# Kernel optimization log

Measured on AMD Instinct MI355X. Metric: run time of the kernel, lower is better.

The kernel has to match this reference:

```python
import jax, jax.numpy as jnp
import numpy as np

# Model dims (DeepSeek-V2-Lite-like MLA)
B, S, DIM, H = 2, 2048, 2048, 16
QR, KVR = 1536, 512          # q_lora_rank, kv_lora_rank
DN, DR, DV = 128, 64, 128    # qk_nope_head_dim, qk_rope_head_dim, v_head_dim
QKD = DN + DR                # qk_head_dim = 192
SCALE = QKD ** -0.5          # max_seq_len == original_seq_len -> no mscale correction
EPS = float(jnp.finfo(jnp.float32).eps)  # torch.nn.RMSNorm default eps


def rmsnorm(x, w):
    return x * jax.lax.rsqrt(jnp.mean(x * x, axis=-1, keepdims=True) + EPS) * w


def rope(x, cos, sin):
    # x: [B, S, H, D]; cos/sin: [S, D//2]. Matches torch.view_as_complex on
    # consecutive (real, imag) pairs, multiply by freqs_cis, flatten back.
    xr, xi = x[..., 0::2], x[..., 1::2]
    c = cos[None, :, None, :]
    s = sin[None, :, None, :]
    yr = xr * c - xi * s
    yi = xr * s + xi * c
    return jnp.stack([yr, yi], axis=-1).reshape(x.shape)


def _xavier(key, out_f, in_f):
    lim = (6.0 / (in_f + out_f)) ** 0.5
    return jax.random.uniform(key, (out_f, in_f), jnp.float32, -lim, lim)


def setup_inputs() -> dict:
    key = jax.random.key(0)
    ks = jax.random.split(key, 8)
    x = jax.random.normal(ks[0], (B, S, DIM), jnp.float32)
    # rotary tables: theta=10000, rope dim = DR
    inv = 1.0 / (10000.0 ** (np.arange(0, DR, 2, dtype=np.float64) / DR))
    ang = np.arange(S, dtype=np.float64)[:, None] * inv[None, :]
    freqs_cos = jnp.asarray(np.cos(ang), jnp.float32)
    freqs_sin = jnp.asarray(np.sin(ang), jnp.float32)
    # causal mask [S, S]: 0 on/below diagonal, -1e9 above
    idx = jnp.arange(S)
    mask = jnp.where(idx[:, None] >= idx[None, :], 0.0, -1e9).astype(jnp.float32)
    return {
        "x": x,
        "freqs_cos": freqs_cos,
        "freqs_sin": freqs_sin,
        "mask": mask,
        "wq_a_w": _xavier(ks[1], QR, DIM), "wq_a_b": jnp.zeros((QR,), jnp.float32),
        "q_norm_w": jnp.ones((QR,), jnp.float32),
        "wq_b_w": _xavier(ks[2], H * QKD, QR), "wq_b_b": jnp.zeros((H * QKD,), jnp.float32),
        "wkv_a_w": _xavier(ks[3], KVR + DR, DIM), "wkv_a_b": jnp.zeros((KVR + DR,), jnp.float32),
        "kv_norm_w": jnp.ones((KVR,), jnp.float32),
        "wkv_b_w": _xavier(ks[4], H * (DN + DV), KVR), "wkv_b_b": jnp.zeros((H * (DN + DV),), jnp.float32),
        "wo_w": _xavier(ks[5], DIM, H * DV), "wo_b": jnp.zeros((DIM,), jnp.float32),
        "start_pos": 0,
    }


def reference(x, freqs_cos, freqs_sin, mask,
              wq_a_w, wq_a_b, q_norm_w, wq_b_w, wq_b_b,
              wkv_a_w, wkv_a_b, kv_norm_w, wkv_b_w, wkv_b_b,
              wo_w, wo_b, start_pos):
    bsz, seqlen, _ = x.shape
    # low-rank Q: wq_b(RMSNorm(wq_a(x)))
    q = rmsnorm(x @ wq_a_w.T + wq_a_b, q_norm_w) @ wq_b_w.T + wq_b_b
    q = q.reshape(bsz, seqlen, H, QKD)
    q_nope, q_pe = q[..., :DN], q[..., DN:]
    q_pe = rope(q_pe, freqs_cos, freqs_sin)
    # low-rank KV
    kv_a = x @ wkv_a_w.T + wkv_a_b               # [B,S,KVR+DR]
    kv_c, k_pe = kv_a[..., :KVR], kv_a[..., KVR:]
    k_pe = rope(k_pe[:, :, None, :], freqs_cos, freqs_sin)   # [B,S,1,DR]
    q = jnp.concatenate([q_nope, q_pe], axis=-1)             # [B,S,H,QKD]
    kv = rmsnorm(kv_c, kv_norm_w) @ wkv_b_w.T + wkv_b_b
    kv = kv.reshape(bsz, seqlen, H, DN + DV)
    k_nope, v = kv[..., :DN], kv[..., DN:]
    k = jnp.concatenate(
        [k_nope, jnp.broadcast_to(k_pe, (bsz, seqlen, H, DR))], axis=-1)
    scores = jnp.einsum('bshd,bthd->bsht', q, k) * SCALE
    scores = scores + mask[None, :, None, :]
    p = jax.nn.softmax(scores.astype(jnp.float32), axis=-1).astype(x.dtype)
    out = jnp.einsum('bsht,bthd->bshd', p, v).reshape(bsz, seqlen, H * DV)
    return out @ wo_w.T + wo_b
```

## Files before the change

### kernel.cpp

```cpp
#include <hip/hip_runtime.h>

#define SLEN 2048
#define NROW 4096
#define NH   16
#define SCALE_QK 0.07216878364870322f
#define RMS_EPS 1.1920928955078125e-07f

typedef __attribute__((ext_vector_type(8))) short bf16x8;
typedef __attribute__((ext_vector_type(4))) float f32x4;

__device__ __forceinline__ float b2f(short s) {
  union { float f; unsigned u; } x; x.u = ((unsigned)(unsigned short)s) << 16; return x.f;
}
__device__ __forceinline__ short f2b(float f) {
  union { float f; unsigned u; } x; x.f = f;
  unsigned r = x.u + 0x7FFFu + ((x.u >> 16) & 1u);
  return (short)(r >> 16);
}

#define GLOAD_LDS16(g, l) __builtin_amdgcn_global_load_lds( \
  (__attribute__((address_space(1))) void*)(g),             \
  (__attribute__((address_space(3))) void*)(l), 16, 0, 0)

__global__ __launch_bounds__(256) void f2b4_kernel(const float* __restrict__ in,
                                                   short* __restrict__ out, int n4) {
  int i = blockIdx.x * 256 + threadIdx.x;
  if (i >= n4) return;
  float4 v = ((const float4*)in)[i];
  short4 o = make_short4(f2b(v.x), f2b(v.y), f2b(v.z), f2b(v.w));
  ((short4*)out)[i] = o;
}

template<int OUT_BF16>
__global__ __launch_bounds__(256)
void gemm_bt_kernel(const short* __restrict__ A, const short* __restrict__ W,
                    const float* __restrict__ bias, void* __restrict__ Cout,
                    int M, int N, int K)
{
  __shared__ short sA[128 * 32];
  __shared__ short sB[128 * 32];
  int nbn = N >> 7;
  int nwg = gridDim.x;
  int wg = blockIdx.x;
  int cpx = nwg >> 3;
  wg = (wg & 7) * cpx + (wg >> 3);
  int bm = wg / nbn, bn = wg % nbn;
  int tid = threadIdx.x, wid = tid >> 6, lane = tid & 63;
  int wr = wid >> 1, wc = wid & 1;
  int lr = lane & 15, lg = lane >> 4;
  int srow = lane >> 2;
  int skk = (lane & 3) * 8;
  f32x4 acc[4][4] = {};
  const size_t baseA = (size_t)bm * 128 * K;
  const size_t baseW = (size_t)bn * 128 * K;

  for (int k0 = 0; k0 < K; k0 += 32) {
#pragma unroll
    for (int i = 0; i < 2; ++i) {
      int c = wid + i * 4;
      int r = c * 16 + srow;
      GLOAD_LDS16(A + baseA + (size_t)r * K + k0 + skk, &sA[c * 512]);
      GLOAD_LDS16(W + baseW + (size_t)r * K + k0 + skk, &sB[c * 512]);
    }
    asm volatile("s_waitcnt vmcnt(0)" ::: "memory");
    __syncthreads();
    bf16x8 av[4], bv[4];
#pragma unroll
    for (int m = 0; m < 4; ++m) av[m] = *(const bf16x8*)&sA[(wr * 64 + m * 16 + lr) * 32 + lg * 8];
#pragma unroll
    for (int n = 0; n < 4; ++n) bv[n] = *(const bf16x8*)&sB[(wc * 64 + n * 16 + lr) * 32 + lg * 8];
#pragma unroll
    for (int m = 0; m < 4; ++m)
#pragma unroll
      for (int n = 0; n < 4; ++n)
        acc[m][n] = __builtin_amdgcn_mfma_f32_16x16x32_bf16(av[m], bv[n], acc[m][n], 0, 0, 0);
    __syncthreads();
  }

  int row0 = bm * 128 + wr * 64, col0 = bn * 128 + wc * 64;
#pragma unroll
  for (int n = 0; n < 4; ++n) {
    int col = col0 + n * 16 + lr;
    float bb = bias[col];
#pragma unroll
    for (int m = 0; m < 4; ++m) {
#pragma unroll
      for (int j = 0; j < 4; ++j) {
        int row = row0 + m * 16 + lg * 4 + j;
        float v = acc[m][n][j] + bb;
        if (OUT_BF16) ((short*)Cout)[(size_t)row * N + col] = f2b(v);
        else          ((float*)Cout)[(size_t)row * N + col] = v;
      }
    }
  }
}

__global__ __launch_bounds__(256)
void norm_rope_kernel(const float* __restrict__ c1, const float* __restrict__ qw,
                      const float* __restrict__ kvw, const float* __restrict__ fcos,
                      const float* __restrict__ fsin, short* __restrict__ qan,
                      short* __restrict__ kvn, short* __restrict__ kpe)
{
  int row = blockIdx.x;
  int s = row & (SLEN - 1);
  const float* r = c1 + (size_t)row * 2176;
  int tid = threadIdx.x, wid = tid >> 6, lane = tid & 63;
  float vq[6], vk[2];
  float sq = 0.f, sk = 0.f;
#pragma unroll
  for (int i = 0; i < 6; ++i) { vq[i] = r[tid + i * 256]; sq += vq[i] * vq[i]; }
#pragma unroll
  for (int i = 0; i < 2; ++i) { vk[i] = r[1536 + tid + i * 256]; sk += vk[i] * vk[i]; }
#pragma unroll
  for (int off = 32; off > 0; off >>= 1) {
    sq += __shfl_xor(sq, off, 64);
    sk += __shfl_xor(sk, off, 64);
  }
  __shared__ float red[2][4];
  if (lane == 0) { red[0][wid] = sq; red[1][wid] = sk; }
  __syncthreads();
  sq = red[0][0] + red[0][1] + red[0][2] + red[0][3];
  sk = red[1][0] + red[1][1] + red[1][2] + red[1][3];
  float rq = rsqrtf(sq * (1.f / 1536.f) + RMS_EPS);
  float rk = rsqrtf(sk * (1.f / 512.f) + RMS_EPS);
#pragma unroll
  for (int i = 0; i < 6; ++i) qan[(size_t)row * 1536 + tid + i * 256] = f2b(vq[i] * rq * qw[tid + i * 256]);
#pragma unroll
  for (int i = 0; i < 2; ++i) kvn[(size_t)row * 512 + tid + i * 256] = f2b(vk[i] * rk * kvw[tid + i * 256]);
  if (tid < 32) {
    float xr = r[2048 + tid * 2], xi = r[2048 + tid * 2 + 1];
    float c = fcos[s * 32 + tid], sn = fsin[s * 32 + tid];
    kpe[(size_t)row * 64 + tid * 2]     = f2b(xr * c - xi * sn);
    kpe[(size_t)row * 64 + tid * 2 + 1] = f2b(xr * sn + xi * c);
  }
}

__global__ __launch_bounds__(256)
void rope_q_kernel(short* __restrict__ qf, const float* __restrict__ fcos,
                   const float* __restrict__ fsin)
{
  int idx = blockIdx.x * 256 + threadIdx.x;
  int pr = idx & 31; int h = (idx >> 5) & 15; int row = idx >> 9;
  int s = row & (SLEN - 1);
  short2* p = (short2*)(qf + (size_t)row * 3072 + h * 192 + 128 + pr * 2);
  short2 v = *p;
  float xr = b2f(v.x), xi = b2f(v.y);
  float c = fcos[s * 32 + pr], sn = fsin[s * 32 + pr];
  v.x = f2b(xr * c - xi * sn);
  v.y = f2b(xr * sn + xi * c);
  *p = v;
}

__global__ __launch_bounds__(256)
void attn_kernel(const short* __restrict__ qf, const short* __restrict__ kvf,
                 const short* __restrict__ kpe, short* __restrict__ obuf)
{
  __shared__ short sK[64 * 200];
  __shared__ short sVt[128 * 72];
  __shared__ short sP[4][16 * 72];
  int bid = blockIdx.x;
  int qt = bid & 31, h = (bid >> 5) & 15, b = bid >> 9;
  int base = b * SLEN;
  int tid = threadIdx.x, wid = tid >> 6, lane = tid & 63;
  int lr = lane & 15, lg = lane >> 4;
  int qrow = base + qt * 64 + wid * 16;

  bf16x8 qfrag[6];
  {
    const short* qp = qf + (size_t)(qrow + lr) * 3072 + h * 192;
#pragma unroll
    for (int kc = 0; kc < 6; ++kc) qfrag[kc] = *(const bf16x8*)(qp + kc * 32 + lg * 8);
  }
  f32x4 oacc[8] = {};
  float m_i[4], l_i[4];
#pragma unroll
  for (int j = 0; j < 4; ++j) { m_i[j] = -1e30f; l_i[j] = 0.f; }
  int srow0 = qt * 64 + wid * 16 + lg * 4;
  int ntiles = qt + 1;
  int str = tid >> 2, sp4 = tid & 3;
  int tpair = tid & 31, d0v = (tid >> 5) * 16;
  short* sPw = sP[wid];

  for (int it = 0; it < ntiles; ++it) {
    int t0 = it * 64;
    {
      const short* src = kvf + (size_t)(base + t0 + str) * 4096 + h * 256 + sp4 * 32;
      short* dst = &sK[str * 200 + sp4 * 32];
#pragma unroll
      for (int i = 0; i < 4; ++i) *(bf16x8*)(dst + i * 8) = *(const bf16x8*)(src + i * 8);
      const short* srcp = kpe + (size_t)(base + t0 + str) * 64 + sp4 * 16;
      short* dstp = &sK[str * 200 + 128 + sp4 * 16];
#pragma unroll
      for (int i = 0; i < 2; ++i) *(bf16x8*)(dstp + i * 8) = *(const bf16x8*)(srcp + i * 8);
      int tv = tpair * 2;
      const short* sv0 = kvf + (size_t)(base + t0 + tv) * 4096 + h * 256 + 128 + d0v;
      const short* sv1 = sv0 + 4096;
      bf16x8 va0 = *(const bf16x8*)(sv0);
      bf16x8 va1 = *(const bf16x8*)(sv0 + 8);
      bf16x8 vb0 = *(const bf16x8*)(sv1);
      bf16x8 vb1 = *(const bf16x8*)(sv1 + 8);
#pragma unroll
      for (int i = 0; i < 8; ++i) {
        unsigned w0 = (unsigned)(unsigned short)va0[i] | ((unsigned)(unsigned short)vb0[i] << 16);
        *((unsigned*)(sVt + (size_t)(d0v + i) * 72) + tpair) = w0;
        unsigned w1 = (unsigned)(unsigned short)va1[i] | ((unsigned)(unsigned short)vb1[i] << 16);
        *((unsigned*)(sVt + (size_t)(d0v + 8 + i) * 72) + tpair) = w1;
      }
    }
    __syncthreads();

    f32x4 sacc[4] = {};
#pragma unroll
    for (int tt = 0; tt < 4; ++tt) {
#pragma unroll
      for (int kc = 0; kc < 6; ++kc) {
        bf16x8 kf = *(const bf16x8*)&sK[(tt * 16 + lr) * 200 + kc * 32 + lg * 8];
        sacc[tt] = __builtin_amdgcn_mfma_f32_16x16x32_bf16(qfrag[kc], kf, sacc[tt], 0, 0, 0);
      }
    }
    float p[4][4], rmax[4];
#pragma unroll
    for (int j = 0; j < 4; ++j) rmax[j] = -1e30f;
#pragma unroll
    for (int tt = 0; tt < 4; ++tt) {
      int t = t0 + tt * 16 + lr;
#pragma unroll
      for (int j = 0; j < 4; ++j) {
        float x = sacc[tt][j] * SCALE_QK;
        if (t > srow0 + j) x = -1e30f;
        p[tt][j] = x;
        rmax[j] = fmaxf(rmax[j], x);
      }
    }
#pragma unroll
    for (int off = 1; off < 16; off <<= 1)
#pragma unroll
      for (int j = 0; j < 4; ++j) rmax[j] = fmaxf(rmax[j], __shfl_xor(rmax[j], off, 64));
    float sf[4], rsum[4];
#pragma unroll
    for (int j = 0; j < 4; ++j) {
      float mn = fmaxf(m_i[j], rmax[j]);
      sf[j] = __expf(m_i[j] - mn);
      m_i[j] = mn;
      rsum[j] = 0.f;
    }
#pragma unroll
    for (int tt = 0; tt < 4; ++tt)
#pragma unroll
      for (int j = 0; j < 4; ++j) {
        float e = __expf(p[tt][j] - m_i[j]);
        p[tt][j] = e;
        rsum[j] += e;
      }
#pragma unroll
    for (int off = 1; off < 16; off <<= 1)
#pragma unroll
      for (int j = 0; j < 4; ++j) rsum[j] += __shfl_xor(rsum[j], off, 64);
#pragma unroll
    for (int j = 0; j < 4; ++j) l_i[j] = l_i[j] * sf[j] + rsum[j];
#pragma unroll
    for (int dt = 0; dt < 8; ++dt)
#pragma unroll
      for (int j = 0; j < 4; ++j) oacc[dt][j] *= sf[j];
#pragma unroll
    for (int tt = 0; tt < 4; ++tt)
#pragma unroll
      for (int j = 0; j < 4; ++j)
        sPw[(lg * 4 + j) * 72 + tt * 16 + lr] = f2b(p[tt][j]);
    asm volatile("s_waitcnt lgkmcnt(0)" ::: "memory");
    bf16x8 pf[2];
#pragma unroll
    for (int kc = 0; kc < 2; ++kc) pf[kc] = *(const bf16x8*)&sPw[lr * 72 + kc * 32 + lg * 8];
#pragma unroll
    for (int dt = 0; dt < 8; ++dt) {
#pragma unroll
      for (int kc = 0; kc < 2; ++kc) {
        bf16x8 vf = *(const bf16x8*)&sVt[(dt * 16 + lr) * 72 + kc * 32 + lg * 8];
        oacc[dt] = __builtin_amdgcn_mfma_f32_16x16x32_bf16(pf[kc], vf, oacc[dt], 0, 0, 0);
      }
    }
    __syncthreads();
  }

  float inv[4];
#pragma unroll
  for (int j = 0; j < 4; ++j) inv[j] = 1.f / l_i[j];
#pragma unroll
  for (int dt = 0; dt < 8; ++dt)
#pragma unroll
    for (int j = 0; j < 4; ++j) {
      int row = qrow + lg * 4 + j;
      obuf[(size_t)row * 2048 + h * 128 + dt * 16 + lr] = f2b(oacc[dt][j] * inv[j]);
    }
}

extern "C" void kernel_launch(void* const* d_in, const int* in_sizes, int n_in,
                              void* d_out, int out_size, void* d_ws, size_t ws_size,
                              hipStream_t stream)
{
  const float* x    = (const float*)d_in[0];
  const float* fcos = (const float*)d_in[1];
  const float* fsin = (const float*)d_in[2];
  const float* wqa   = (const float*)d_in[4];
  const float* wqab  = (const float*)d_in[5];
  const float* qnw   = (const float*)d_in[6];
  const float* wqb   = (const float*)d_in[7];
  const float* wqbb  = (const float*)d_in[8];
  const float* wkva  = (const float*)d_in[9];
  const float* wkvab = (const float*)d_in[10];
  const float* kvnw  = (const float*)d_in[11];
  const float* wkvb  = (const float*)d_in[12];
  const float* wkvbb = (const float*)d_in[13];
  const float* wo    = (const float*)d_in[14];
  const float* wob   = (const float*)d_in[15];
  float* out = (float*)d_out;

  char* ws = (char*)d_ws;
  size_t off = 0;
  auto alloc = [&](size_t bytes) {
    char* p = ws + off;
    off += (bytes + 255) & ~(size_t)255;
    return p;
  };
  short* xb     = (short*)alloc(4096ull * 2048 * 2);
  short* w1     = (short*)alloc(2176ull * 2048 * 2);
  float* b1     = (float*)alloc(2176 * 4);
  short* wqb16  = (short*)alloc(3072ull * 1536 * 2);
  short* wkvb16 = (short*)alloc(4096ull * 512 * 2);
  short* wob16  = (short*)alloc(2048ull * 2048 * 2);
  float* c1     = (float*)alloc(4096ull * 2176 * 4);
  short* qan    = (short*)alloc(4096ull * 1536 * 2);
  short* kvn    = (short*)alloc(4096ull * 512 * 2);
  short* kpe    = (short*)alloc(4096ull * 64 * 2);
  short* qfull  = (short*)alloc(4096ull * 3072 * 2);
  short* kvfull = (short*)alloc(4096ull * 4096 * 2);
  short* obuf   = (short*)alloc(4096ull * 2048 * 2);
  (void)ws_size; (void)in_sizes; (void)n_in; (void)out_size;

  f2b4_kernel<<<8192, 256, 0, stream>>>(x, xb, 2097152);
  f2b4_kernel<<<3072, 256, 0, stream>>>(wqa, w1, 786432);
  f2b4_kernel<<<1152, 256, 0, stream>>>(wkva, w1 + 1536ull * 2048, 294912);
  hipMemsetAsync(w1 + 2112ull * 2048, 0, 64ull * 2048 * 2, stream);
  hipMemcpyAsync(b1, wqab, 1536 * 4, hipMemcpyDeviceToDevice, stream);
  hipMemcpyAsync(b1 + 1536, wkvab, 576 * 4, hipMemcpyDeviceToDevice, stream);
  hipMemsetAsync(b1 + 2112, 0, 64 * 4, stream);
  f2b4_kernel<<<4608, 256, 0, stream>>>(wqb, wqb16, 1179648);
  f2b4_kernel<<<2048, 256, 0, stream>>>(wkvb, wkvb16, 524288);
  f2b4_kernel<<<4096, 256, 0, stream>>>(wo, wob16, 1048576);

  gemm_bt_kernel<0><<<544, 256, 0, stream>>>(xb, w1, b1, c1, 4096, 2176, 2048);
  norm_rope_kernel<<<4096, 256, 0, stream>>>(c1, qnw, kvnw, fcos, fsin, qan, kvn, kpe);
  gemm_bt_kernel<1><<<768, 256, 0, stream>>>(qan, wqb16, wqbb, qfull, 4096, 3072, 1536);
  gemm_bt_kernel<1><<<1024, 256, 0, stream>>>(kvn, wkvb16, wkvbb, kvfull, 4096, 4096, 512);
  rope_q_kernel<<<8192, 256, 0, stream>>>(qfull, fcos, fsin);
  attn_kernel<<<1024, 256, 0, stream>>>(qfull, kvfull, kpe, obuf);
  gemm_bt_kernel<0><<<512, 256, 0, stream>>>(obuf, wob16, wob, out, 4096, 2048, 2048);
}
```

Baseline: 671.7 us.

## Pair complementary causal query tiles per block and add lazy softmax rescaling

Each attention block now handles two query tiles, i and 31-i, so every block does about the same causal work. Each K/V tile loaded into shared memory is reused for both query tiles. The block index is also remapped (bid&7 interleave), and the online softmax now rescales the accumulators only when the running max grows by more than a threshold. Together these balance causal load, halve K/V tile traffic per query, and skip most rescale multiplies. The cost is doubled register state per thread (two Q fragments and two accumulators) under a launch_bounds occupancy hint of 2, which risks spills. The grid also shrinks to 512 blocks.

New measurement: 563.6 us. -16.1%, faster.

```diff
diff --git a/kernel.cpp b/kernel.cpp
--- a/kernel.cpp
+++ b/kernel.cpp
@@ -151,47 +151,111 @@
   *p = v;
 }
 
-__global__ __launch_bounds__(256)
+__device__ __forceinline__ void softmax16(f32x4* sacc, float p[4][4], float* m_i,
+                                          float* l_i, f32x4* oacc, int t0, int srow0, int lr)
+{
+  float rmax[4];
+#pragma unroll
+  for (int j = 0; j < 4; ++j) rmax[j] = -1e30f;
+#pragma unroll
+  for (int tt = 0; tt < 4; ++tt) {
+    int t = t0 + tt * 16 + lr;
+#pragma unroll
+    for (int j = 0; j < 4; ++j) {
+      float x = sacc[tt][j] * SCALE_QK;
+      if (t > srow0 + j) x = -1e30f;
+      p[tt][j] = x;
+      rmax[j] = fmaxf(rmax[j], x);
+    }
+  }
+#pragma unroll
+  for (int off = 1; off < 16; off <<= 1)
+#pragma unroll
+    for (int j = 0; j < 4; ++j) rmax[j] = fmaxf(rmax[j], __shfl_xor(rmax[j], off, 64));
+  bool grow = false;
+#pragma unroll
+  for (int j = 0; j < 4; ++j) grow = grow || (rmax[j] > m_i[j] + 8.f);
+  if (__any((int)grow)) {
+    float sf[4];
+#pragma unroll
+    for (int j = 0; j < 4; ++j) {
+      float mn = fmaxf(m_i[j], rmax[j]);
+      sf[j] = __expf(m_i[j] - mn);
+      m_i[j] = mn;
+      l_i[j] *= sf[j];
+    }
+#pragma unroll
+    for (int dt = 0; dt < 8; ++dt)
+#pragma unroll
+      for (int j = 0; j < 4; ++j) oacc[dt][j] *= sf[j];
+  }
+  float rsum[4] = {0.f, 0.f, 0.f, 0.f};
+#pragma unroll
+  for (int tt = 0; tt < 4; ++tt)
+#pragma unroll
+    for (int j = 0; j < 4; ++j) {
+      float e = __expf(p[tt][j] - m_i[j]);
+      p[tt][j] = e;
+      rsum[j] += e;
+    }
+#pragma unroll
+  for (int off = 1; off < 16; off <<= 1)
+#pragma unroll
+    for (int j = 0; j < 4; ++j) rsum[j] += __shfl_xor(rsum[j], off, 64);
+#pragma unroll
+  for (int j = 0; j < 4; ++j) l_i[j] += rsum[j];
+}
+
+__global__ __launch_bounds__(256, 2)
 void attn_kernel(const short* __restrict__ qf, const short* __restrict__ kvf,
                  const short* __restrict__ kpe, short* __restrict__ obuf)
 {
   __shared__ short sK[64 * 200];
   __shared__ short sVt[128 * 72];
-  __shared__ short sP[4][16 * 72];
+  __shared__ short sPA[4][16 * 72];
+  __shared__ short sPB[4][16 * 72];
   int bid = blockIdx.x;
-  int qt = bid & 31, h = (bid >> 5) & 15, b = bid >> 9;
+  bid = (bid & 7) * 64 + (bid >> 3);
+  int i = bid & 15, h = (bid >> 4) & 15, b = bid >> 8;
+  int qtA = i, qtB = 31 - i;
   int base = b * SLEN;
   int tid = threadIdx.x, wid = tid >> 6, lane = tid & 63;
   int lr = lane & 15, lg = lane >> 4;
-  int qrow = base + qt * 64 + wid * 16;
-
-  bf16x8 qfrag[6];
+  int qrowA = base + qtA * 64 + wid * 16;
+  int qrowB = base + qtB * 64 + wid * 16;
+
+  bf16x8 qfragA[6], qfragB[6];
   {
-    const short* qp = qf + (size_t)(qrow + lr) * 3072 + h * 192;
-#pragma unroll
-    for (int kc = 0; kc < 6; ++kc) qfrag[kc] = *(const bf16x8*)(qp + kc * 32 + lg * 8);
-  }
-  f32x4 oacc[8] = {};
-  float m_i[4], l_i[4];
-#pragma unroll
-  for (int j = 0; j < 4; ++j) { m_i[j] = -1e30f; l_i[j] = 0.f; }
-  int srow0 = qt * 64 + wid * 16 + lg * 4;
-  int ntiles = qt + 1;
+    const short* qpA = qf + (size_t)(qrowA + lr) * 3072 + h * 192;
+    const short* qpB = qf + (size_t)(qrowB + lr) * 3072 + h * 192;
+#pragma unroll
+    for (int kc = 0; kc < 6; ++kc) {
+      qfragA[kc] = *(const bf16x8*)(qpA + kc * 32 + lg * 8);
+      qfragB[kc] = *(const bf16x8*)(qpB + kc * 32 + lg * 8);
+    }
+  }
+  f32x4 oaccA[8] = {}, oaccB[8] = {};
+  float mA[4], lA[4], mB[4], lB[4];
+#pragma unroll
+  for (int j = 0; j < 4; ++j) { mA[j] = mB[j] = -1e30f; lA[j] = lB[j] = 0.f; }
+  int srow0A = qtA * 64 + wid * 16 + lg * 4;
+  int srow0B = qtB * 64 + wid * 16 + lg * 4;
   int str = tid >> 2, sp4 = tid & 3;
   int tpair = tid & 31, d0v = (tid >> 5) * 16;
-  short* sPw = sP[wid];
-
-  for (int it = 0; it < ntiles; ++it) {
+  short* sPAw = sPA[wid];
+  short* sPBw = sPB[wid];
+
+  for (int it = 0; it <= qtB; ++it) {
     int t0 = it * 64;
     {
       const short* src = kvf + (size_t)(base + t0 + str) * 4096 + h * 256 + sp4 * 32;
       short* dst = &sK[str * 200 + sp4 * 32];
 #pragma unroll
-      for (int i = 0; i < 4; ++i) *(bf16x8*)(dst + i * 8) = *(const bf16x8*)(src + i * 8);
+      for (int k = 0; k < 4; ++k) *(bf16x8*)(dst + k * 8) = *(const bf16x8*)(src + k * 8);
       const short* srcp = kpe + (size_t)(base + t0 + str) * 64 + sp4 * 16;
       short* dstp = &sK[str * 200 + 128 + sp4 * 16];
 #pragma unroll
-      for (int i = 0; i < 2; ++i) *(bf16x8*)(dstp + i * 8) = *(const bf16x8*)(srcp + i * 8);
+      for (int k = 0; k < 2; ++k) *(bf16x8*)(dstp + k * 8) = *(const bf16x8*)(srcp + k * 8);
       int tv = tpair * 2;
       const short* sv0 = kvf + (size_t)(base + t0 + tv) * 4096 + h * 256 + 128 + d0v;
       const short* sv1 = sv0 + 4096;
@@ -200,97 +264,91 @@
       bf16x8 vb0 = *(const bf16x8*)(sv1);
       bf16x8 vb1 = *(const bf16x8*)(sv1 + 8);
 #pragma unroll
-      for (int i = 0; i < 8; ++i) {
-        unsigned w0 = (unsigned)(unsigned short)va0[i] | ((unsigned)(unsigned short)vb0[i] << 16);
-        *((unsigned*)(sVt + (size_t)(d0v + i) * 72) + tpair) = w0;
-        unsigned w1 = (unsigned)(unsigned short)va1[i] | ((unsigned)(unsigned short)vb1[i] << 16);
-        *((unsigned*)(sVt + (size_t)(d0v + 8 + i) * 72) + tpair) = w1;
+      for (int k = 0; k < 8; ++k) {
+        unsigned w0 = (unsigned)(unsigned short)va0[k] | ((unsigned)(unsigned short)vb0[k] << 16);
+        *((unsigned*)(sVt + (size_t)(d0v + k) * 72) + tpair) = w0;
+        unsigned w1 = (unsigned)(unsigned short)va1[k] | ((unsigned)(unsigned short)vb1[k] << 16);
+        *((unsigned*)(sVt + (size_t)(d0v + 8 + k) * 72) + tpair) = w1;
       }
     }
     __syncthreads();
-
-    f32x4 sacc[4] = {};
-#pragma unroll
-    for (int tt = 0; tt < 4; ++tt) {
+    bool doA = (it <= qtA);
+
+    f32x4 saccB[4] = {};
+#pragma unroll
+    for (int tt = 0; tt < 4; ++tt)
 #pragma unroll
       for (int kc = 0; kc < 6; ++kc) {
         bf16x8 kf = *(const bf16x8*)&sK[(tt * 16 + lr) * 200 + kc * 32 + lg * 8];
-        sacc[tt] = __builtin_amdgcn_mfma_f32_16x16x32_bf16(qfrag[kc], kf, sacc[tt], 0, 0, 0);
+        saccB[tt] = __builtin_amdgcn_mfma_f32_16x16x32_bf16(qfragB[kc], kf, saccB[tt], 0, 0, 0);
       }
-    }
-    float p[4][4], rmax[4];
-#pragma unroll
-    for (int j = 0; j < 4; ++j) rmax[j] = -1e30f;
-#pragma unroll
-    for (int tt = 0; tt < 4; ++tt) {
-      int t = t0 + tt * 16 + lr;
-#pragma unroll
-      for (int j = 0; j < 4; ++j) {
-        float x = sacc[tt][j] * SCALE_QK;
-        if (t > srow0 + j) x = -1e30f;
-        p[tt][j] = x;
-        rmax[j] = fmaxf(rmax[j], x);
-      }
-    }
-#pragma unroll
-    for (int off = 1; off < 16; off <<= 1)
-#pragma unroll
-      for (int j = 0; j < 4; ++j) rmax[j] = fmaxf(rmax[j], __shfl_xor(rmax[j], off, 64));
-    float sf[4], rsum[4];
+    f32x4 saccA[4] = {};
+    if (doA) {
+#pragma unroll
+      for (int tt = 0; tt < 4; ++tt)
+#pragma unroll
+        for (int kc = 0; kc < 6; ++kc) {
+          bf16x8 kf = *(const bf16x8*)&sK[(tt * 16 + lr) * 200 + kc * 32 + lg * 8];
+          saccA[tt] = __builtin_amdgcn_mfma_f32_16x16x32_bf16(qfragA[kc], kf, saccA[tt], 0, 0, 0);
+        }
+    }
+    {
+      float pB[4][4];
+      softmax16(saccB, pB, mB, lB, oaccB, t0, srow0B, lr);
+#pragma unroll
+      for (int tt = 0; tt < 4; ++tt)
+#pragma unroll
+        for (int j = 0; j < 4; ++j)
+          sPBw[(lg * 4 + j) * 72 + tt * 16 + lr] = f2b(pB[tt][j]);
+    }
+    if (doA) {
+      float pA[4][4];
+      softmax16(saccA, pA, mA, lA, oaccA, t0, srow0A, lr);
+#pragma unroll
+      for (int tt = 0; tt < 4; ++tt)
+#pragma unroll
+        for (int j = 0; j < 4; ++j)
+          sPAw[(lg * 4 + j) * 72 + tt * 16 + lr] = f2b(pA[tt][j]);
+    }
+    asm volatile("s_waitcnt lgkmcnt(0)" ::: "memory");
+    {
+      bf16x8 pf[2];
+#pragma unroll
+      for (int kc = 0; kc < 2; ++kc) pf[kc] = *(const bf16x8*)&sPBw[lr * 72 + kc * 32 + lg * 8];
+#pragma unroll
+      for (int dt = 0; dt < 8; ++dt)
+#pragma unroll
+        for (int kc = 0; kc < 2; ++kc) {
+          bf16x8 vf = *(const bf16x8*)&sVt[(dt * 16 + lr) * 72 + kc * 32 + lg * 8];
+          oaccB[dt] = __builtin_amdgcn_mfma_f32_16x16x32_bf16(pf[kc], vf, oaccB[dt], 0, 0, 0);
+        }
+    }
+    if (doA) {
+      bf16x8 pf[2];
+#pragma unroll
+      for (int kc = 0; kc < 2; ++kc) pf[kc] = *(const bf16x8*)&sPAw[lr * 72 + kc * 32 + lg * 8];
+#pragma unroll
+      for (int dt = 0; dt < 8; ++dt)
+#pragma unroll
+        for (int kc = 0; kc < 2; ++kc) {
+          bf16x8 vf = *(const bf16x8*)&sVt[(dt * 16 + lr) * 72 + kc * 32 + lg * 8];
+          oaccA[dt] = __builtin_amdgcn_mfma_f32_16x16x32_bf16(pf[kc], vf, oaccA[dt], 0, 0, 0);
+        }
+    }
+    __syncthreads();
+  }
+
+  float invA[4], invB[4];
+#pragma unroll
+  for (int j = 0; j < 4; ++j) { invA[j] = 1.f / lA[j]; invB[j] = 1.f / lB[j]; }
+#pragma unroll
+  for (int dt = 0; dt < 8; ++dt)
 #pragma unroll
     for (int j = 0; j < 4; ++j) {
-      float mn = fmaxf(m_i[j], rmax[j]);
-      sf[j] = __expf(m_i[j] - mn);
-      m_i[j] = mn;
-      rsum[j] = 0.f;
-    }
-#pragma unroll
-    for (int tt = 0; tt < 4; ++tt)
-#pragma unroll
-      for (int j = 0; j < 4; ++j) {
-        float e = __expf(p[tt][j] - m_i[j]);
-        p[tt][j] = e;
-        rsum[j] += e;
-      }
-#pragma unroll
-    for (int off = 1; off < 16; off <<= 1)
-#pragma unroll
-      for (int j = 0; j < 4; ++j) rsum[j] += __shfl_xor(rsum[j], off, 64);
-#pragma unroll
-    for (int j = 0; j < 4; ++j) l_i[j] = l_i[j] * sf[j] + rsum[j];
-#pragma unroll
-    for (int dt = 0; dt < 8; ++dt)
-#pragma unroll
-      for (int j = 0; j < 4; ++j) oacc[dt][j] *= sf[j];
-#pragma unroll
-    for (int tt = 0; tt < 4; ++tt)
-#pragma unroll
-      for (int j = 0; j < 4; ++j)
-        sPw[(lg * 4 + j) * 72 + tt * 16 + lr] = f2b(p[tt][j]);
-    asm volatile("s_waitcnt lgkmcnt(0)" ::: "memory");
-    bf16x8 pf[2];
-#pragma unroll
-    for (int kc = 0; kc < 2; ++kc) pf[kc] = *(const bf16x8*)&sPw[lr * 72 + kc * 32 + lg * 8];
-#pragma unroll
-    for (int dt = 0; dt < 8; ++dt) {
-#pragma unroll
-      for (int kc = 0; kc < 2; ++kc) {
-        bf16x8 vf = *(const bf16x8*)&sVt[(dt * 16 + lr) * 72 + kc * 32 + lg * 8];
-        oacc[dt] = __builtin_amdgcn_mfma_f32_16x16x32_bf16(pf[kc], vf, oacc[dt], 0, 0, 0);
-      }
-    }
-    __syncthreads();
-  }
-
-  float inv[4];
-#pragma unroll
-  for (int j = 0; j < 4; ++j) inv[j] = 1.f / l_i[j];
-#pragma unroll
-  for (int dt = 0; dt < 8; ++dt)
-#pragma unroll
-    for (int j = 0; j < 4; ++j) {
-      int row = qrow + lg * 4 + j;
-      obuf[(size_t)row * 2048 + h * 128 + dt * 16 + lr] = f2b(oacc[dt][j] * inv[j]);
+      int rowA = qrowA + lg * 4 + j;
+      int rowB = qrowB + lg * 4 + j;
+      obuf[(size_t)rowA * 2048 + h * 128 + dt * 16 + lr] = f2b(oaccA[dt][j] * invA[j]);
+      obuf[(size_t)rowB * 2048 + h * 128 + dt * 16 + lr] = f2b(oaccB[dt][j] * invB[j]);
     }
 }
 
@@ -353,6 +411,6 @@
   gemm_bt_kernel<1><<<768, 256, 0, stream>>>(qan, wqb16, wqbb, qfull, 4096, 3072, 1536);
   gemm_bt_kernel<1><<<1024, 256, 0, stream>>>(kvn, wkvb16, wkvbb, kvfull, 4096, 4096, 512);
   rope_q_kernel<<<8192, 256, 0, stream>>>(qfull, fcos, fsin);
-  attn_kernel<<<1024, 256, 0, stream>>>(qfull, kvfull, kpe, obuf);
+  attn_kernel<<<512, 256, 0, stream>>>(qfull, kvfull, kpe, obuf);
   gemm_bt_kernel<0><<<512, 256, 0, stream>>>(obuf, wob16, wob, out, 4096, 2048, 2048);
 }
```
